# Kernel optimization log

Hardware: AMD Instinct MI355X
Metric: run time of the kernel (lower is better)

The kernel has to match this reference:

```python
import jax, jax.numpy as jnp
import numpy as np
from jax import lax

NUM_CLASS = 1000
LOW_DIM = 128
PROTO_M = 0.99
B_UPD = 1024
B_SIM = 65536
EPS = 1e-12  # F.normalize eps


def setup_inputs() -> dict:
    key = jax.random.key(0)
    k1, k2, k3, k4 = jax.random.split(key, 4)
    pred_feat = jax.random.normal(k1, (B_UPD, LOW_DIM), dtype=jnp.float32)
    pseudo_label = jax.random.randint(k2, (B_UPD,), 0, NUM_CLASS, dtype=jnp.int32)
    prototypes = jax.random.normal(k3, (NUM_CLASS, LOW_DIM), dtype=jnp.float32)
    feat = jax.random.normal(k4, (B_SIM, LOW_DIM), dtype=jnp.float32)
    return {"pred_feat": pred_feat, "pseudo_label": pseudo_label,
            "prototypes": prototypes, "feat": feat}


def _update_proto(prototypes, pred_feat, pseudo_label, m=PROTO_M):
    # Sequential per-sample EMA scatter (order matters when labels repeat),
    # expressed as a lax.scan recurrence over the batch.
    def step(protos, xl):
        f, lab = xl
        new = m * protos[lab] + (1.0 - m) * f
        return protos.at[lab].set(new), None
    prototypes, _ = lax.scan(step, prototypes, (pred_feat, pseudo_label))
    # F.normalize(p=2, dim=1): x / max(||x||_2, eps)
    norms = jnp.sqrt(jnp.sum(prototypes * prototypes, axis=1, keepdims=True))
    return prototypes / jnp.maximum(norms, EPS)


def reference(pred_feat, pseudo_label, prototypes, feat):
    protos = _update_proto(prototypes, pred_feat, pseudo_label)
    # cal_proto_sim: feat @ prototypes.T (prototypes detached in original)
    protos = lax.stop_gradient(protos)
    sim = jnp.matmul(feat, protos.T)  # [B_SIM, NUM_CLASS]
    return sim
```

## Files before the change

kernel.cpp:

```cpp
#include <hip/hip_runtime.h>
#include <hip/hip_bf16.h>
#include <cstdint>
#include <cstddef>

#define NUM_CLASS 1000
#define NPAD      1024
#define LOW_DIM   128
#define B_UPD     1024
#define B_SIM     65536

typedef short bf16x8 __attribute__((ext_vector_type(8)));
typedef float f32x4  __attribute__((ext_vector_type(4)));

__device__ __forceinline__ unsigned short f2bf(float f) {
  union { float f; unsigned u; } a; a.f = f;
  unsigned u = a.u;
  return (unsigned short)((u + 0x7fffu + ((u >> 16) & 1u)) >> 16);
}

__global__ void proto_update_kernel(const float* __restrict__ pred_feat,
                                    const int*   __restrict__ labels,
                                    const float* __restrict__ protos_in,
                                    unsigned short* __restrict__ protos_sw) {
  int c = blockIdx.x;
  int d = threadIdx.x;
  float p = 0.0f;
  if (c < NUM_CLASS) {
    p = protos_in[c * LOW_DIM + d];
    #pragma unroll 4
    for (int k = 0; k < B_UPD / 64; ++k) {
      int lab = labels[k * 64 + (d & 63)];
      unsigned long long m = __ballot(lab == c);
      while (m) {
        int b = __builtin_ctzll(m);
        m &= (m - 1);
        p = 0.99f * p + 0.01f * pred_feat[(size_t)(k * 64 + b) * LOW_DIM + d];
      }
    }
  }
  float sq = p * p;
  #pragma unroll
  for (int o = 1; o < 64; o <<= 1) sq += __shfl_xor(sq, o, 64);
  __shared__ float wsum[2];
  if ((d & 63) == 0) wsum[d >> 6] = sq;
  __syncthreads();
  float total = wsum[0] + wsum[1];
  unsigned short v = f2bf(p / fmaxf(sqrtf(total), 1e-12f));
  int g = c >> 4, r = c & 15, kk = d >> 5, j = (d >> 3) & 3, e = d & 7;
  protos_sw[(size_t)((g * 4 + kk) * 64 + j * 16 + r) * 8 + e] = v;
}

#define BM   32
#define TPB2 512

__global__ __launch_bounds__(TPB2, 4)
void gemm_sim_kernel(const float* __restrict__ A,
                     const unsigned short* __restrict__ Bsw,
                     float* __restrict__ C) {
  __shared__ alignas(16) unsigned char Als[BM * 256];
  int t  = threadIdx.x;
  int m0 = blockIdx.x * BM;

  {
    int row = t >> 4, c8 = t & 15;
    const float4* s = reinterpret_cast<const float4*>(A + (size_t)(m0 + row) * LOW_DIM + c8 * 8);
    float4 v0 = s[0], v1 = s[1];
    uint4 q;
    q.x = f2bf(v0.x) | ((unsigned)f2bf(v0.y) << 16);
    q.y = f2bf(v0.z) | ((unsigned)f2bf(v0.w) << 16);
    q.z = f2bf(v1.x) | ((unsigned)f2bf(v1.y) << 16);
    q.w = f2bf(v1.z) | ((unsigned)f2bf(v1.w) << 16);
    *reinterpret_cast<uint4*>(Als + row * 256 + ((c8 * 16) ^ ((row & 7) << 4))) = q;
  }
  __syncthreads();

  int lane = t & 63;
  int w    = t >> 6;
  int lr   = lane & 15;
  int lkb  = (lane >> 4) * 16;

  f32x4 acc[2][8];
  #pragma unroll
  for (int m = 0; m < 2; ++m)
    #pragma unroll
    for (int n = 0; n < 8; ++n)
      acc[m][n] = (f32x4){0.f, 0.f, 0.f, 0.f};

  #pragma unroll
  for (int kk = 0; kk < 4; ++kk) {
    int kb = kk * 64 + lkb;
    bf16x8 af[2];
    #pragma unroll
    for (int m = 0; m < 2; ++m) {
      int row = m * 16 + lr;
      af[m] = *reinterpret_cast<const bf16x8*>(Als + row * 256 + (kb ^ ((row & 7) << 4)));
    }
    #pragma unroll
    for (int n = 0; n < 8; ++n) {
      int g = w * 8 + n;
      bf16x8 bf = *reinterpret_cast<const bf16x8*>(
          Bsw + ((size_t)(g * 4 + kk) * 64 + lane) * 8);
      #pragma unroll
      for (int m = 0; m < 2; ++m)
        acc[m][n] = __builtin_amdgcn_mfma_f32_16x16x32_bf16(af[m], bf, acc[m][n], 0, 0, 0);
    }
  }

  int colbase = w * 128 + lr;
  #pragma unroll
  for (int m = 0; m < 2; ++m) {
    size_t rowbase = (size_t)(m0 + m * 16 + (lane >> 4) * 4) * NUM_CLASS;
    #pragma unroll
    for (int r = 0; r < 4; ++r) {
      float* Crow = C + rowbase + (size_t)r * NUM_CLASS + colbase;
      #pragma unroll
      for (int n = 0; n < 8; ++n) {
        int col = colbase + n * 16;
        if (col < NUM_CLASS)
          Crow[n * 16] = acc[m][n][r];
      }
    }
  }
}

extern "C" void kernel_launch(void* const* d_in, const int* in_sizes, int n_in,
                              void* d_out, int out_size, void* d_ws, size_t ws_size,
                              hipStream_t stream) {
  const float* pred_feat = (const float*)d_in[0];
  const int*   labels    = (const int*)d_in[1];
  const float* protos    = (const float*)d_in[2];
  const float* feat      = (const float*)d_in[3];
  float* out = (float*)d_out;

  unsigned short* protos_sw = (unsigned short*)d_ws;

  proto_update_kernel<<<NPAD, 128, 0, stream>>>(pred_feat, labels, protos, protos_sw);
  gemm_sim_kernel<<<B_SIM / BM, TPB2, 0, stream>>>(feat, protos_sw, out);
}
```

Baseline: 79.48 us.

## Swap MFMA operands for vectorized float4 output stores, halve row tile

Swaps the A and B operands of the MFMA so each lane holds four consecutive output columns of one row, which allows 16-byte vector stores to C instead of scattered scalar stores. The row tile drops from 32 to 16 per block, and the launch bounds target 6 blocks per CU to raise occupancy. The cost is twice as many blocks, each reloading the full prototype matrix for half the work, so prototype reads per output row double.

After: 114.1 us. 1.44x slower.

```diff
diff --git a/kernel.cpp b/kernel.cpp
--- a/kernel.cpp
+++ b/kernel.cpp
@@ -50,10 +50,10 @@
   protos_sw[(size_t)((g * 4 + kk) * 64 + j * 16 + r) * 8 + e] = v;
 }
 
-#define BM   32
+#define BM   16
 #define TPB2 512
 
-__global__ __launch_bounds__(TPB2, 4)
+__global__ __launch_bounds__(TPB2, 6)
 void gemm_sim_kernel(const float* __restrict__ A,
                      const unsigned short* __restrict__ Bsw,
                      float* __restrict__ C) {
@@ -62,15 +62,12 @@
   int m0 = blockIdx.x * BM;
 
   {
-    int row = t >> 4, c8 = t & 15;
-    const float4* s = reinterpret_cast<const float4*>(A + (size_t)(m0 + row) * LOW_DIM + c8 * 8);
-    float4 v0 = s[0], v1 = s[1];
-    uint4 q;
-    q.x = f2bf(v0.x) | ((unsigned)f2bf(v0.y) << 16);
-    q.y = f2bf(v0.z) | ((unsigned)f2bf(v0.w) << 16);
-    q.z = f2bf(v1.x) | ((unsigned)f2bf(v1.y) << 16);
-    q.w = f2bf(v1.z) | ((unsigned)f2bf(v1.w) << 16);
-    *reinterpret_cast<uint4*>(Als + row * 256 + ((c8 * 16) ^ ((row & 7) << 4))) = q;
+    int row = t >> 5, c4 = t & 31;
+    float4 v = *reinterpret_cast<const float4*>(A + (size_t)(m0 + row) * LOW_DIM + c4 * 4);
+    uint2 q;
+    q.x = f2bf(v.x) | ((unsigned)f2bf(v.y) << 16);
+    q.y = f2bf(v.z) | ((unsigned)f2bf(v.w) << 16);
+    *reinterpret_cast<uint2*>(Als + row * 256 + ((c4 * 8) ^ ((row & 7) << 4))) = q;
   }
   __syncthreads();
 
@@ -79,46 +76,32 @@
   int lr   = lane & 15;
   int lkb  = (lane >> 4) * 16;
 
-  f32x4 acc[2][8];
+  f32x4 acc[8];
   #pragma unroll
-  for (int m = 0; m < 2; ++m)
-    #pragma unroll
-    for (int n = 0; n < 8; ++n)
-      acc[m][n] = (f32x4){0.f, 0.f, 0.f, 0.f};
+  for (int n = 0; n < 8; ++n)
+    acc[n] = (f32x4){0.f, 0.f, 0.f, 0.f};
 
   #pragma unroll
   for (int kk = 0; kk < 4; ++kk) {
-    int kb = kk * 64 + lkb;
-    bf16x8 af[2];
-    #pragma unroll
-    for (int m = 0; m < 2; ++m) {
-      int row = m * 16 + lr;
-      af[m] = *reinterpret_cast<const bf16x8*>(Als + row * 256 + (kb ^ ((row & 7) << 4)));
-    }
+    int kb  = kk * 64 + lkb;
+    int row = lr;
+    bf16x8 af = *reinterpret_cast<const bf16x8*>(Als + row * 256 + (kb ^ ((row & 7) << 4)));
     #pragma unroll
     for (int n = 0; n < 8; ++n) {
       int g = w * 8 + n;
       bf16x8 bf = *reinterpret_cast<const bf16x8*>(
           Bsw + ((size_t)(g * 4 + kk) * 64 + lane) * 8);
-      #pragma unroll
-      for (int m = 0; m < 2; ++m)
-        acc[m][n] = __builtin_amdgcn_mfma_f32_16x16x32_bf16(af[m], bf, acc[m][n], 0, 0, 0);
+      acc[n] = __builtin_amdgcn_mfma_f32_16x16x32_bf16(bf, af, acc[n], 0, 0, 0);
     }
   }
 
-  int colbase = w * 128 + lr;
+  size_t rowoff = (size_t)(m0 + lr) * NUM_CLASS;
+  int q = (lane >> 4) * 4;
   #pragma unroll
-  for (int m = 0; m < 2; ++m) {
-    size_t rowbase = (size_t)(m0 + m * 16 + (lane >> 4) * 4) * NUM_CLASS;
-    #pragma unroll
-    for (int r = 0; r < 4; ++r) {
-      float* Crow = C + rowbase + (size_t)r * NUM_CLASS + colbase;
-      #pragma unroll
-      for (int n = 0; n < 8; ++n) {
-        int col = colbase + n * 16;
-        if (col < NUM_CLASS)
-          Crow[n * 16] = acc[m][n][r];
-      }
+  for (int n = 0; n < 8; ++n) {
+    int col = w * 128 + n * 16 + q;
+    if (col < NUM_CLASS) {
+      *reinterpret_cast<f32x4*>(C + rowoff + col) = acc[n];
     }
   }
 }
```
